# Kernel optimization log

Hardware: AMD Instinct MI355X
Metric: run time of the kernel (lower is better)

Reference implementation:

```python
import jax, jax.numpy as jnp
import numpy as np

WS = 7          # window size
SHIFT = 3       # shift size = ws // 2
HEADS = 16
N = WS * WS     # tokens per window


def _rel_pos_index(ws):
    coords = np.stack(np.meshgrid(np.arange(ws), np.arange(ws), indexing='ij')).reshape(2, -1)
    rel = (coords[:, :, None] - coords[:, None, :]).transpose(1, 2, 0)
    rel[:, :, 0] += ws - 1
    rel[:, :, 1] += ws - 1
    rel[:, :, 0] *= 2 * ws - 1
    return rel.sum(-1)  # [N, N] int


def _attn_mask(H, W, ws, s):
    # Swin cyclic-shift mask: windows spanning the wrap boundary get -100 on
    # cross-region pairs so softmax zeroes them out.
    img = np.zeros((H, W), np.float32)
    cnt = 0
    for hs in (slice(0, -ws), slice(-ws, -s), slice(-s, None)):
        for wsl in (slice(0, -ws), slice(-ws, -s), slice(-s, None)):
            img[hs, wsl] = cnt
            cnt += 1
    mw = img.reshape(H // ws, ws, W // ws, ws).transpose(0, 2, 1, 3).reshape(-1, ws * ws)
    diff = mw[:, None, :] - mw[:, :, None]
    return np.where(diff != 0, np.float32(-100.0), np.float32(0.0))  # [nW, N, N]


def _window_partition(x, ws):
    B, H, W, C = x.shape
    x = x.reshape(B, H // ws, ws, W // ws, ws, C).transpose(0, 1, 3, 2, 4, 5)
    return x.reshape(-1, ws * ws, C)  # [B*nW, N, C]


def _window_reverse(x, ws, B, H, W):
    C = x.shape[-1]
    x = x.reshape(B, H // ws, W // ws, ws, ws, C).transpose(0, 1, 3, 2, 4, 5)
    return x.reshape(B, H, W, C)


def setup_inputs() -> dict:
    key = jax.random.key(0)
    ks = jax.random.split(key, 5)
    B, H, W, C = 16, 56, 56, 512
    x = jax.random.normal(ks[0], (B, H, W, C), jnp.float32)
    qkv_w = jax.random.normal(ks[1], (C, 3 * C), jnp.float32) * 0.02
    qkv_b = jnp.zeros((3 * C,), jnp.float32)
    proj_w = jax.random.normal(ks[2], (C, C), jnp.float32) * 0.02
    proj_b = jnp.zeros((C,), jnp.float32)
    rel_bias_table = jax.random.normal(ks[3], ((2 * WS - 1) ** 2, HEADS), jnp.float32) * 0.02
    return {"x": x, "qkv_w": qkv_w, "qkv_b": qkv_b,
            "proj_w": proj_w, "proj_b": proj_b, "rel_bias_table": rel_bias_table}


def reference(x, qkv_w, qkv_b, proj_w, proj_b, rel_bias_table):
    B, H, W, C = x.shape
    d = C // HEADS
    scale = jnp.float32(d) ** -0.5

    rel_idx = jnp.asarray(_rel_pos_index(WS))                 # [N, N]
    mask = jnp.asarray(_attn_mask(H, W, WS, SHIFT))           # [nW, N, N]
    nW = mask.shape[0]

    shortcut = x
    # cyclic shift
    xs = jnp.roll(x, shift=(-SHIFT, -SHIFT), axis=(1, 2))
    xw = _window_partition(xs, WS)                            # [B*nW, N, C]

    qkv = xw @ qkv_w + qkv_b                                  # [B*nW, N, 3C]
    qkv = qkv.reshape(-1, N, 3, HEADS, d).transpose(2, 0, 3, 1, 4)
    q, k, v = qkv[0], qkv[1], qkv[2]                          # each [B*nW, h, N, d]

    attn = jnp.einsum('whnd,whmd->whnm', q * scale, k)        # [B*nW, h, N, N]
    # gathered relative-position bias [h, N, N]
    bias = rel_bias_table[rel_idx.reshape(-1)].reshape(N, N, HEADS).transpose(2, 0, 1)
    attn = attn + bias[None]
    # shift mask, broadcast per window
    attn = attn.reshape(B, nW, HEADS, N, N) + mask[None, :, None]
    attn = jax.nn.softmax(attn.reshape(-1, HEADS, N, N), axis=-1)

    out = jnp.einsum('whnm,whmd->whnd', attn, v)              # [B*nW, h, N, d]
    out = out.transpose(0, 2, 1, 3).reshape(-1, N, C)
    out = out @ proj_w + proj_b

    out = _window_reverse(out, WS, B, H, W)
    out = jnp.roll(out, shift=(SHIFT, SHIFT), axis=(1, 2))
    return shortcut + out
```

## Files before the change

### kernel.cpp

```cpp
#include <hip/hip_runtime.h>
#include <stdint.h>

typedef unsigned short u16;
typedef unsigned int   u32;

typedef __bf16 bf16x8 __attribute__((ext_vector_type(8)));
typedef float  f32x4  __attribute__((ext_vector_type(4)));

__device__ __forceinline__ float bf2f(u16 h) {
    return __uint_as_float(((u32)h) << 16);
}
__device__ __forceinline__ u16 f2bf(float f) {
    u32 u = __float_as_uint(f);
    u += 0x7FFFu + ((u >> 16) & 1u);
    return (u16)(u >> 16);
}

#define GLOAD_LDS16(g, l)                                                     \
    __builtin_amdgcn_global_load_lds(                                         \
        (const __attribute__((address_space(1))) void*)(g),                   \
        (__attribute__((address_space(3))) void*)(l), 16, 0, 0)

__global__ __launch_bounds__(256) void cvt_f32_bf16(const float* __restrict__ in,
                                                    u16* __restrict__ out) {
    int i = blockIdx.x * 256 + threadIdx.x;
    const float4* p = (const float4*)in + (size_t)i * 2;
    float4 a = p[0], b = p[1];
    union { u16 s[8]; uint4 v; } o;
    o.s[0] = f2bf(a.x); o.s[1] = f2bf(a.y); o.s[2] = f2bf(a.z); o.s[3] = f2bf(a.w);
    o.s[4] = f2bf(b.x); o.s[5] = f2bf(b.y); o.s[6] = f2bf(b.z); o.s[7] = f2bf(b.w);
    ((uint4*)out)[i] = o.v;
}

__global__ void transpose_cvt(const float* __restrict__ in, u16* __restrict__ out,
                              int R, int Cc) {
    __shared__ float tile[32][33];
    int c0 = blockIdx.x * 32, r0 = blockIdx.y * 32;
    int tx = threadIdx.x, ty = threadIdx.y;
    tile[ty][tx] = in[(size_t)(r0 + ty) * Cc + c0 + tx];
    __syncthreads();
    out[(size_t)(c0 + ty) * R + r0 + tx] = f2bf(tile[tx][ty]);
}

__global__ __launch_bounds__(64) void build_bias(const float* __restrict__ table,
                                                 float* __restrict__ biasL) {
    int cls = blockIdx.x >> 4;
    int h   = blockIdx.x & 15;
    int lane = threadIdx.x;
    int quad = lane >> 4, l16 = lane & 15;
    int eh = cls >> 1, ew = cls & 1;
    float* base = biasL + (size_t)(cls * 16 + h) * 4096;
#pragma unroll
    for (int mi = 0; mi < 4; mi++) {
#pragma unroll
        for (int ni = 0; ni < 4; ni++) {
            float4 v;
            float* vp = &v.x;
#pragma unroll
            for (int r = 0; r < 4; r++) {
                int m = mi * 16 + quad * 4 + r;
                int c = ni * 16 + l16;
                float b;
                if (c >= 49)      b = -1e9f;
                else if (m >= 49) b = 0.f;
                else {
                    int ty = m / 7, tx = m % 7, jy = c / 7, jx = c % 7;
                    b = table[((ty - jy + 6) * 13 + (tx - jx + 6)) * 16 + h];
                    int ridr = (eh ? (ty < 4 ? 1 : 2) : 0) * 3 + (ew ? (tx < 4 ? 1 : 2) : 0);
                    int ridc = (eh ? (jy < 4 ? 1 : 2) : 0) * 3 + (ew ? (jx < 4 ? 1 : 2) : 0);
                    if (ridr != ridc) b -= 100.f;
                }
                vp[r] = b;
            }
            ((float4*)base)[((mi * 4 + ni) * 4 + quad) * 16 + l16] = v;
        }
    }
}

template <bool OUT_F32>
__global__ __launch_bounds__(256) void gemm_bt(
    const u16* __restrict__ A, const u16* __restrict__ Bt,
    const float* __restrict__ bias, const float* __restrict__ res,
    void* __restrict__ Cout, int M, int N, int K)
{
    __shared__ __align__(16) char smem[17408];
    u16* As = (u16*)smem;
    u16* Bs = (u16*)(smem + 8192);

    const int t    = threadIdx.x;
    const int lane = t & 63;
    const int w    = t >> 6;
    const int wm   = w >> 1, wn = w & 1;
    const int quad = lane >> 4, l16 = lane & 15;

    const size_t m0 = (size_t)blockIdx.y * 128;
    const size_t n0 = (size_t)blockIdx.x * 128;

    const u16* Ab = A + m0 * K;
    const u16* Bb = Bt + n0 * K;

    const int rA0 = t >> 2;
    const int cA0 = (t & 3) * 8;

    f32x4 acc[4][4];
    const f32x4 fzero = {0.f, 0.f, 0.f, 0.f};
#pragma unroll
    for (int i = 0; i < 4; i++)
#pragma unroll
        for (int j = 0; j < 4; j++) acc[i][j] = fzero;

    for (int k0 = 0; k0 < K; k0 += 32) {
        const u16* ga0 = Ab + (size_t)rA0 * K + k0 + cA0;
        const u16* ga1 = ga0 + (size_t)64 * K;
        const u16* gb0 = Bb + (size_t)rA0 * K + k0 + cA0;
        const u16* gb1 = gb0 + (size_t)64 * K;
        GLOAD_LDS16(ga0, As + t * 8);
        GLOAD_LDS16(ga1, As + t * 8 + 2048);
        GLOAD_LDS16(gb0, Bs + t * 8);
        GLOAD_LDS16(gb1, Bs + t * 8 + 2048);
        __syncthreads();

        bf16x8 a[4], b[4];
#pragma unroll
        for (int mi = 0; mi < 4; mi++)
            a[mi] = *(const bf16x8*)(As + (wm * 64 + mi * 16 + l16) * 32 + quad * 8);
#pragma unroll
        for (int ni = 0; ni < 4; ni++)
            b[ni] = *(const bf16x8*)(Bs + (wn * 64 + ni * 16 + l16) * 32 + quad * 8);
#pragma unroll
        for (int mi = 0; mi < 4; mi++)
#pragma unroll
            for (int ni = 0; ni < 4; ni++)
                acc[mi][ni] = __builtin_amdgcn_mfma_f32_16x16x32_bf16(
                    a[mi], b[ni], acc[mi][ni], 0, 0, 0);
        __syncthreads();
    }

    float* scr = (float*)smem + w * 1088;
    float bv[4];
#pragma unroll
    for (int ni = 0; ni < 4; ni++)
        bv[ni] = bias[n0 + wn * 64 + ni * 16 + l16];

    const size_t colb = n0 + wn * 64 + quad * 16;
#pragma unroll
    for (int mi = 0; mi < 4; mi++) {
#pragma unroll
        for (int ni = 0; ni < 4; ni++)
#pragma unroll
            for (int r = 0; r < 4; r++)
                scr[(quad * 4 + r) * 68 + ni * 16 + l16] = acc[mi][ni][r] + bv[ni];
        __builtin_amdgcn_s_waitcnt(0);

        const size_t row = m0 + wm * 64 + mi * 16 + l16;
        const float4* sp = (const float4*)(scr + l16 * 68 + quad * 16);
        float4 v0 = sp[0], v1 = sp[1], v2 = sp[2], v3 = sp[3];

        if (OUT_F32) {
            const float4* rp = (const float4*)(res + row * N + colb);
            float4 r0 = rp[0], r1 = rp[1], r2 = rp[2], r3 = rp[3];
            v0.x += r0.x; v0.y += r0.y; v0.z += r0.z; v0.w += r0.w;
            v1.x += r1.x; v1.y += r1.y; v1.z += r1.z; v1.w += r1.w;
            v2.x += r2.x; v2.y += r2.y; v2.z += r2.z; v2.w += r2.w;
            v3.x += r3.x; v3.y += r3.y; v3.z += r3.z; v3.w += r3.w;
            float4* op = (float4*)((float*)Cout + row * N + colb);
            op[0] = v0; op[1] = v1; op[2] = v2; op[3] = v3;
        } else {
            union { u16 s[8]; uint4 q; } p0, p1;
            p0.s[0] = f2bf(v0.x); p0.s[1] = f2bf(v0.y); p0.s[2] = f2bf(v0.z); p0.s[3] = f2bf(v0.w);
            p0.s[4] = f2bf(v1.x); p0.s[5] = f2bf(v1.y); p0.s[6] = f2bf(v1.z); p0.s[7] = f2bf(v1.w);
            p1.s[0] = f2bf(v2.x); p1.s[1] = f2bf(v2.y); p1.s[2] = f2bf(v2.z); p1.s[3] = f2bf(v2.w);
            p1.s[4] = f2bf(v3.x); p1.s[5] = f2bf(v3.y); p1.s[6] = f2bf(v3.z); p1.s[7] = f2bf(v3.w);
            uint4* op = (uint4*)((u16*)Cout + row * N + colb);
            op[0] = p0.q; op[1] = p1.q;
        }
        __builtin_amdgcn_s_waitcnt(0);
    }
}

__global__ __launch_bounds__(64) void attn_kernel(
    const u16* __restrict__ qkv, const float* __restrict__ biasL,
    u16* __restrict__ O)
{
    __shared__ __align__(16) u16 Ps[64 * 72];
    __shared__ __align__(16) u16 Vts[32 * 72];

    const int wid = blockIdx.x >> 4;
    const int h   = blockIdx.x & 15;
    const int b   = wid >> 6;
    const int wy  = (wid >> 3) & 7;
    const int wx  = wid & 7;
    const int cls = ((wy == 7) ? 2 : 0) + ((wx == 7) ? 1 : 0);
    const int lane = threadIdx.x;
    const int quad = lane >> 4, l16 = lane & 15;

    auto tokOf = [&](int m) -> size_t {
        int tt = m < 49 ? m : 48;
        int ty = tt / 7, tx = tt - ty * 7;
        int ho = wy * 7 + ty + 3; if (ho >= 56) ho -= 56;
        int wo = wx * 7 + tx + 3; if (wo >= 56) wo -= 56;
        return ((size_t)b * 56 + ho) * 56 + wo;
    };

    {
        size_t tok = tokOf(lane);
        const uint4* vs = (const uint4*)(qkv + tok * 1536 + 1024 + h * 32);
        union { uint4 u4[4]; u16 s[32]; } vb;
        vb.u4[0] = vs[0]; vb.u4[1] = vs[1]; vb.u4[2] = vs[2]; vb.u4[3] = vs[3];
#pragma unroll
        for (int d = 0; d < 32; d++) Vts[d * 72 + lane] = vb.s[d];
    }

    bf16x8 aq[4], bk[4];
#pragma unroll
    for (int i = 0; i < 4; i++) {
        size_t tok = tokOf(i * 16 + l16);
        const u16* base = qkv + tok * 1536 + h * 32 + quad * 8;
        aq[i] = *(const bf16x8*)base;
        bk[i] = *(const bf16x8*)(base + 512);
    }

    f32x4 acc[4][4];
    {
        const f32x4 fz = {0.f, 0.f, 0.f, 0.f};
#pragma unroll
        for (int mi = 0; mi < 4; mi++)
#pragma unroll
            for (int ni = 0; ni < 4; ni++)
                acc[mi][ni] = __builtin_amdgcn_mfma_f32_16x16x32_bf16(
                    aq[mi], bk[ni], fz, 0, 0, 0);
    }

    {
        const float scale = 0.17677669529663687f;
        const float* bp = biasL + (size_t)(cls * 16 + h) * 4096;
#pragma unroll
        for (int mi = 0; mi < 4; mi++)
#pragma unroll
            for (int ni = 0; ni < 4; ni++) {
                float4 bvv = ((const float4*)bp)[((mi * 4 + ni) * 4 + quad) * 16 + l16];
                const float* bvp = &bvv.x;
#pragma unroll
                for (int r = 0; r < 4; r++)
                    acc[mi][ni][r] = acc[mi][ni][r] * scale + bvp[r];
            }
    }

    float rinv[4][4];
    {
#pragma unroll
        for (int mi = 0; mi < 4; mi++)
#pragma unroll
            for (int r = 0; r < 4; r++) {
                float m0 = fmaxf(fmaxf(acc[mi][0][r], acc[mi][1][r]),
                                 fmaxf(acc[mi][2][r], acc[mi][3][r]));
                m0 = fmaxf(m0, __shfl_xor(m0, 1, 64));
                m0 = fmaxf(m0, __shfl_xor(m0, 2, 64));
                m0 = fmaxf(m0, __shfl_xor(m0, 4, 64));
                m0 = fmaxf(m0, __shfl_xor(m0, 8, 64));
                float e0 = __expf(acc[mi][0][r] - m0);
                float e1 = __expf(acc[mi][1][r] - m0);
                float e2 = __expf(acc[mi][2][r] - m0);
                float e3 = __expf(acc[mi][3][r] - m0);
                acc[mi][0][r] = e0; acc[mi][1][r] = e1;
                acc[mi][2][r] = e2; acc[mi][3][r] = e3;
                float s0 = (e0 + e1) + (e2 + e3);
                s0 += __shfl_xor(s0, 1, 64);
                s0 += __shfl_xor(s0, 2, 64);
                s0 += __shfl_xor(s0, 4, 64);
                s0 += __shfl_xor(s0, 8, 64);
                rinv[mi][r] = __builtin_amdgcn_rcpf(s0);
            }
    }

#pragma unroll
    for (int mi = 0; mi < 4; mi++)
#pragma unroll
        for (int ni = 0; ni < 4; ni++)
#pragma unroll
            for (int r = 0; r < 4; r++)
                Ps[(mi * 16 + quad * 4 + r) * 72 + ni * 16 + l16] =
                    f2bf(acc[mi][ni][r]);
    __syncthreads();

#pragma unroll
    for (int mi = 0; mi < 4; mi++) {
        f32x4 c0 = {0.f, 0.f, 0.f, 0.f}, c1 = {0.f, 0.f, 0.f, 0.f};
#pragma unroll
        for (int ks = 0; ks < 2; ks++) {
            bf16x8 a = *(const bf16x8*)(Ps + (mi * 16 + l16) * 72 + ks * 32 + quad * 8);
            bf16x8 b0 = *(const bf16x8*)(Vts + l16 * 72 + ks * 32 + quad * 8);
            bf16x8 b1 = *(const bf16x8*)(Vts + (16 + l16) * 72 + ks * 32 + quad * 8);
            c0 = __builtin_amdgcn_mfma_f32_16x16x32_bf16(a, b0, c0, 0, 0, 0);
            c1 = __builtin_amdgcn_mfma_f32_16x16x32_bf16(a, b1, c1, 0, 0, 0);
        }
#pragma unroll
        for (int r = 0; r < 4; r++) {
            int m = mi * 16 + quad * 4 + r;
            if (m < 49) {
                int ty = m / 7, tx = m - ty * 7;
                int ho = wy * 7 + ty + 3; if (ho >= 56) ho -= 56;
                int wo = wx * 7 + tx + 3; if (wo >= 56) wo -= 56;
                size_t tok = ((size_t)b * 56 + ho) * 56 + wo;
                u16* op = O + tok * 512 + h * 32 + l16;
                op[0]  = f2bf(c0[r] * rinv[mi][r]);
                op[16] = f2bf(c1[r] * rinv[mi][r]);
            }
        }
    }
}

extern "C" void kernel_launch(void* const* d_in, const int* in_sizes, int n_in,
                              void* d_out, int out_size, void* d_ws, size_t ws_size,
                              hipStream_t stream)
{
    const float* x      = (const float*)d_in[0];
    const float* qkv_w  = (const float*)d_in[1];
    const float* qkv_b  = (const float*)d_in[2];
    const float* proj_w = (const float*)d_in[3];
    const float* proj_b = (const float*)d_in[4];
    const float* table  = (const float*)d_in[5];
    float* out = (float*)d_out;

    const int M  = 16 * 56 * 56;
    const int Cd = 512, C3 = 1536;

    char* ws = (char*)d_ws;
    u16* QKV  = (u16*)ws;
    u16* Xb   = (u16*)(ws + (size_t)M * C3 * 2);
    u16* Obuf = Xb;
    u16* Wt1  = (u16*)(ws + (size_t)M * C3 * 2 + (size_t)M * Cd * 2);
    u16* Wt2  = Wt1 + (size_t)C3 * Cd;
    float* biasL = (float*)Wt1;

    cvt_f32_bf16<<<(M * Cd) / 2048, 256, 0, stream>>>(x, Xb);

    dim3 tb(32, 32);
    transpose_cvt<<<dim3(C3 / 32, Cd / 32), tb, 0, stream>>>(qkv_w, Wt1, Cd, C3);
    transpose_cvt<<<dim3(Cd / 32, Cd / 32), tb, 0, stream>>>(proj_w, Wt2, Cd, Cd);

    gemm_bt<false><<<dim3(C3 / 128, M / 128), 256, 0, stream>>>(
        Xb, Wt1, qkv_b, nullptr, QKV, M, C3, Cd);

    build_bias<<<dim3(64), 64, 0, stream>>>(table, biasL);

    attn_kernel<<<dim3(1024 * 16), 64, 0, stream>>>(QKV, biasL, Obuf);

    gemm_bt<true><<<dim3(Cd / 128, M / 128), 256, 0, stream>>>(
        Obuf, Wt2, proj_b, x, out, M, Cd, Cd);
}
```

Measured before the change: 478.9 us.

## Replace 128x128 GEMM with double-buffered 256x256 swizzled pipelined GEMM

Replaces the simple single-buffered 128x128 bf16 GEMM with a 256x256-tile, 512-thread kernel that uses a 64-wide K step. It double-buffers LDS across half-tiles and interleaves global-to-LDS prefetch with MFMA phases under s_setprio. LDS reads use an XOR swizzle to avoid bank conflicts, and workgroup IDs are remapped for L2 locality. The goal is to hide load latency and raise arithmetic intensity for both the QKV and projection GEMMs. The cost is 128KB of LDS per block, which limits occupancy, and fragile manual vmcnt waits and barriers.

After: 453.7 us. -5.3%, faster.

```diff
diff --git a/kernel.cpp b/kernel.cpp
--- a/kernel.cpp
+++ b/kernel.cpp
@@ -78,91 +78,190 @@
 }
 
 template <bool OUT_F32>
-__global__ __launch_bounds__(256) void gemm_bt(
+__global__ __launch_bounds__(512, 2) void gemm256(
     const u16* __restrict__ A, const u16* __restrict__ Bt,
     const float* __restrict__ bias, const float* __restrict__ res,
-    void* __restrict__ Cout, int M, int N, int K)
+    void* __restrict__ Cout, int M, int N, int K, int GX)
 {
-    __shared__ __align__(16) char smem[17408];
-    u16* As = (u16*)smem;
-    u16* Bs = (u16*)(smem + 8192);
+    __shared__ __align__(16) char smem[131072];
+    char* AsB = smem;
+    char* BsB = smem + 65536;
+
+    const int nwg = (int)gridDim.x;
+    int wg = (int)blockIdx.x;
+    wg = (wg & 7) * (nwg >> 3) + (wg >> 3);
+    const int bx = wg % GX;
+    const int by = wg / GX;
+    const size_t m0 = (size_t)by * 256;
+    const size_t n0 = (size_t)bx * 256;
 
     const int t    = threadIdx.x;
     const int lane = t & 63;
     const int w    = t >> 6;
-    const int wm   = w >> 1, wn = w & 1;
+    const int wm   = w >> 2, wn = w & 3;
     const int quad = lane >> 4, l16 = lane & 15;
-
-    const size_t m0 = (size_t)blockIdx.y * 128;
-    const size_t n0 = (size_t)blockIdx.x * 128;
-
-    const u16* Ab = A + m0 * K;
-    const u16* Bb = Bt + n0 * K;
-
-    const int rA0 = t >> 2;
-    const int cA0 = (t & 3) * 8;
-
-    f32x4 acc[4][4];
-    const f32x4 fzero = {0.f, 0.f, 0.f, 0.f};
-#pragma unroll
-    for (int i = 0; i < 4; i++)
-#pragma unroll
-        for (int j = 0; j < 4; j++) acc[i][j] = fzero;
-
-    for (int k0 = 0; k0 < K; k0 += 32) {
-        const u16* ga0 = Ab + (size_t)rA0 * K + k0 + cA0;
-        const u16* ga1 = ga0 + (size_t)64 * K;
-        const u16* gb0 = Bb + (size_t)rA0 * K + k0 + cA0;
-        const u16* gb1 = gb0 + (size_t)64 * K;
-        GLOAD_LDS16(ga0, As + t * 8);
-        GLOAD_LDS16(ga1, As + t * 8 + 2048);
-        GLOAD_LDS16(gb0, Bs + t * 8);
-        GLOAD_LDS16(gb1, Bs + t * 8 + 2048);
-        __syncthreads();
-
-        bf16x8 a[4], b[4];
-#pragma unroll
-        for (int mi = 0; mi < 4; mi++)
-            a[mi] = *(const bf16x8*)(As + (wm * 64 + mi * 16 + l16) * 32 + quad * 8);
-#pragma unroll
-        for (int ni = 0; ni < 4; ni++)
-            b[ni] = *(const bf16x8*)(Bs + (wn * 64 + ni * 16 + l16) * 32 + quad * 8);
-#pragma unroll
-        for (int mi = 0; mi < 4; mi++)
-#pragma unroll
-            for (int ni = 0; ni < 4; ni++)
-                acc[mi][ni] = __builtin_amdgcn_mfma_f32_16x16x32_bf16(
-                    a[mi], b[ni], acc[mi][ni], 0, 0, 0);
-        __syncthreads();
-    }
-
-    float* scr = (float*)smem + w * 1088;
+    const int xr   = l16 & 7;
+    const int cb   = (quad ^ xr) * 16;
+
+    const int r0  = t >> 3;
+    const int s8  = t & 7;
+    const int swz = (s8 ^ (r0 & 7)) * 8;
+    const u16* Ag0 = A  + (m0 + r0) * K + swz;
+    const u16* Bg0 = Bt + (n0 + r0) * K + swz;
+    const size_t j64K = (size_t)64 * K;
+    const int lo0 = t * 16, lo1 = t * 16 + 8192;
+
+    auto stageA = [&](int bf, int half, int ktt) {
+        char* d = AsB + bf * 32768 + half * 16384;
+        const u16* g = Ag0 + (size_t)half * 128 * K + ktt * 64;
+        GLOAD_LDS16(g, d + lo0);
+        GLOAD_LDS16(g + j64K, d + lo1);
+    };
+    auto stageB = [&](int bf, int half, int ktt) {
+        char* d = BsB + bf * 32768 + half * 16384;
+        const u16* g = Bg0 + (size_t)half * 128 * K + ktt * 64;
+        GLOAD_LDS16(g, d + lo0);
+        GLOAD_LDS16(g + j64K, d + lo1);
+    };
+
+    f32x4 acc[8][4];
+    const f32x4 fz = {0.f, 0.f, 0.f, 0.f};
+#pragma unroll
+    for (int i = 0; i < 8; i++)
+#pragma unroll
+        for (int j = 0; j < 4; j++) acc[i][j] = fz;
+
+    const int NT = K >> 6;
+
+    stageA(0, 0, 0); stageA(0, 1, 0); stageB(0, 0, 0); stageB(0, 1, 0);
+    stageB(1, 0, 1); stageA(1, 0, 1);
+    asm volatile("s_waitcnt vmcnt(4)" ::: "memory");
+    __builtin_amdgcn_s_barrier();
+
+    for (int kt = 0; kt < NT; ++kt) {
+        const int buf = kt & 1;
+        const char* Ab  = AsB + buf * 32768 + wm * 16384 + l16 * 128;
+        const char* Bb  = BsB + buf * 32768 + (wn >> 1) * 16384 + (wn & 1) * 8192 + l16 * 128;
+        const char* pA0 = Ab + cb;
+        const char* pA1 = Ab + (cb ^ 64);
+        const char* pB0 = Bb + cb;
+        const char* pB1 = Bb + (cb ^ 64);
+
+        bf16x8 a[4][2], b0[2][2], b1[2][2];
+
+#pragma unroll
+        for (int mi = 0; mi < 4; mi++) {
+            a[mi][0] = *(const bf16x8*)(pA0 + mi * 2048);
+            a[mi][1] = *(const bf16x8*)(pA1 + mi * 2048);
+        }
+#pragma unroll
+        for (int nj = 0; nj < 2; nj++) {
+            b0[nj][0] = *(const bf16x8*)(pB0 + nj * 2048);
+            b0[nj][1] = *(const bf16x8*)(pB1 + nj * 2048);
+        }
+        if (kt + 1 < NT) stageA((kt + 1) & 1, 1, kt + 1);
+        __builtin_amdgcn_s_barrier();
+        asm volatile("s_waitcnt lgkmcnt(0)" ::: "memory");
+        __builtin_amdgcn_s_setprio(1);
+#pragma unroll
+        for (int mi = 0; mi < 4; mi++)
+#pragma unroll
+            for (int nj = 0; nj < 2; nj++) {
+                acc[mi][nj] = __builtin_amdgcn_mfma_f32_16x16x32_bf16(
+                    a[mi][0], b0[nj][0], acc[mi][nj], 0, 0, 0);
+                acc[mi][nj] = __builtin_amdgcn_mfma_f32_16x16x32_bf16(
+                    a[mi][1], b0[nj][1], acc[mi][nj], 0, 0, 0);
+            }
+        __builtin_amdgcn_s_setprio(0);
+        __builtin_amdgcn_s_barrier();
+
+#pragma unroll
+        for (int nj = 0; nj < 2; nj++) {
+            b1[nj][0] = *(const bf16x8*)(pB0 + 4096 + nj * 2048);
+            b1[nj][1] = *(const bf16x8*)(pB1 + 4096 + nj * 2048);
+        }
+        if (kt + 1 < NT) stageB((kt + 1) & 1, 1, kt + 1);
+        __builtin_amdgcn_s_barrier();
+        asm volatile("s_waitcnt lgkmcnt(0)" ::: "memory");
+        __builtin_amdgcn_s_setprio(1);
+#pragma unroll
+        for (int mi = 0; mi < 4; mi++)
+#pragma unroll
+            for (int nj = 0; nj < 2; nj++) {
+                acc[mi][2 + nj] = __builtin_amdgcn_mfma_f32_16x16x32_bf16(
+                    a[mi][0], b1[nj][0], acc[mi][2 + nj], 0, 0, 0);
+                acc[mi][2 + nj] = __builtin_amdgcn_mfma_f32_16x16x32_bf16(
+                    a[mi][1], b1[nj][1], acc[mi][2 + nj], 0, 0, 0);
+            }
+        __builtin_amdgcn_s_setprio(0);
+        __builtin_amdgcn_s_barrier();
+
+#pragma unroll
+        for (int mi = 0; mi < 4; mi++) {
+            a[mi][0] = *(const bf16x8*)(pA0 + 8192 + mi * 2048);
+            a[mi][1] = *(const bf16x8*)(pA1 + 8192 + mi * 2048);
+        }
+        if (kt + 2 < NT) stageB(buf, 0, kt + 2);
+        __builtin_amdgcn_s_barrier();
+        asm volatile("s_waitcnt lgkmcnt(0)" ::: "memory");
+        __builtin_amdgcn_s_setprio(1);
+#pragma unroll
+        for (int mi = 0; mi < 4; mi++)
+#pragma unroll
+            for (int nj = 0; nj < 2; nj++) {
+                acc[4 + mi][2 + nj] = __builtin_amdgcn_mfma_f32_16x16x32_bf16(
+                    a[mi][0], b1[nj][0], acc[4 + mi][2 + nj], 0, 0, 0);
+                acc[4 + mi][2 + nj] = __builtin_amdgcn_mfma_f32_16x16x32_bf16(
+                    a[mi][1], b1[nj][1], acc[4 + mi][2 + nj], 0, 0, 0);
+            }
+        __builtin_amdgcn_s_setprio(0);
+        __builtin_amdgcn_s_barrier();
+
+        if (kt + 2 < NT) stageA(buf, 0, kt + 2);
+        __builtin_amdgcn_s_barrier();
+        __builtin_amdgcn_s_setprio(1);
+#pragma unroll
+        for (int mi = 0; mi < 4; mi++)
+#pragma unroll
+            for (int nj = 0; nj < 2; nj++) {
+                acc[4 + mi][nj] = __builtin_amdgcn_mfma_f32_16x16x32_bf16(
+                    a[mi][0], b0[nj][0], acc[4 + mi][nj], 0, 0, 0);
+                acc[4 + mi][nj] = __builtin_amdgcn_mfma_f32_16x16x32_bf16(
+                    a[mi][1], b0[nj][1], acc[4 + mi][nj], 0, 0, 0);
+            }
+        __builtin_amdgcn_s_setprio(0);
+        if (kt < NT - 2) asm volatile("s_waitcnt vmcnt(4)" ::: "memory");
+        else             asm volatile("s_waitcnt vmcnt(0)" ::: "memory");
+        __builtin_amdgcn_s_barrier();
+    }
+
+    float* scr = (float*)(void*)smem + w * 1088;
     float bv[4];
 #pragma unroll
-    for (int ni = 0; ni < 4; ni++)
-        bv[ni] = bias[n0 + wn * 64 + ni * 16 + l16];
+    for (int nj = 0; nj < 4; nj++)
+        bv[nj] = bias[n0 + wn * 64 + nj * 16 + l16];
 
     const size_t colb = n0 + wn * 64 + quad * 16;
 #pragma unroll
-    for (int mi = 0; mi < 4; mi++) {
-#pragma unroll
-        for (int ni = 0; ni < 4; ni++)
+    for (int mi = 0; mi < 8; mi++) {
+#pragma unroll
+        for (int nj = 0; nj < 4; nj++)
 #pragma unroll
             for (int r = 0; r < 4; r++)
-                scr[(quad * 4 + r) * 68 + ni * 16 + l16] = acc[mi][ni][r] + bv[ni];
+                scr[(quad * 4 + r) * 68 + nj * 16 + l16] = acc[mi][nj][r] + bv[nj];
         __builtin_amdgcn_s_waitcnt(0);
 
-        const size_t row = m0 + wm * 64 + mi * 16 + l16;
+        const size_t row = m0 + wm * 128 + mi * 16 + l16;
         const float4* sp = (const float4*)(scr + l16 * 68 + quad * 16);
         float4 v0 = sp[0], v1 = sp[1], v2 = sp[2], v3 = sp[3];
 
         if (OUT_F32) {
             const float4* rp = (const float4*)(res + row * N + colb);
-            float4 r0 = rp[0], r1 = rp[1], r2 = rp[2], r3 = rp[3];
-            v0.x += r0.x; v0.y += r0.y; v0.z += r0.z; v0.w += r0.w;
-            v1.x += r1.x; v1.y += r1.y; v1.z += r1.z; v1.w += r1.w;
-            v2.x += r2.x; v2.y += r2.y; v2.z += r2.z; v2.w += r2.w;
-            v3.x += r3.x; v3.y += r3.y; v3.z += r3.z; v3.w += r3.w;
+            float4 r0v = rp[0], r1v = rp[1], r2v = rp[2], r3v = rp[3];
+            v0.x += r0v.x; v0.y += r0v.y; v0.z += r0v.z; v0.w += r0v.w;
+            v1.x += r1v.x; v1.y += r1v.y; v1.z += r1v.z; v1.w += r1v.w;
+            v2.x += r2v.x; v2.y += r2v.y; v2.z += r2v.z; v2.w += r2v.w;
+            v3.x += r3v.x; v3.y += r3v.y; v3.z += r3v.z; v3.w += r3v.w;
             float4* op = (float4*)((float*)Cout + row * N + colb);
             op[0] = v0; op[1] = v1; op[2] = v2; op[3] = v3;
         } else {
@@ -222,13 +321,13 @@
 
     f32x4 acc[4][4];
     {
-        const f32x4 fz = {0.f, 0.f, 0.f, 0.f};
+        const f32x4 fzz = {0.f, 0.f, 0.f, 0.f};
 #pragma unroll
         for (int mi = 0; mi < 4; mi++)
 #pragma unroll
             for (int ni = 0; ni < 4; ni++)
                 acc[mi][ni] = __builtin_amdgcn_mfma_f32_16x16x32_bf16(
-                    aq[mi], bk[ni], fz, 0, 0, 0);
+                    aq[mi], bk[ni], fzz, 0, 0, 0);
     }
 
     {
@@ -339,13 +438,13 @@
     transpose_cvt<<<dim3(C3 / 32, Cd / 32), tb, 0, stream>>>(qkv_w, Wt1, Cd, C3);
     transpose_cvt<<<dim3(Cd / 32, Cd / 32), tb, 0, stream>>>(proj_w, Wt2, Cd, Cd);
 
-    gemm_bt<false><<<dim3(C3 / 128, M / 128), 256, 0, stream>>>(
-        Xb, Wt1, qkv_b, nullptr, QKV, M, C3, Cd);
+    gemm256<false><<<dim3((M / 256) * (C3 / 256)), 512, 0, stream>>>(
+        Xb, Wt1, qkv_b, nullptr, QKV, M, C3, Cd, C3 / 256);
 
     build_bias<<<dim3(64), 64, 0, stream>>>(table, biasL);
 
     attn_kernel<<<dim3(1024 * 16), 64, 0, stream>>>(QKV, biasL, Obuf);
 
-    gemm_bt<true><<<dim3(Cd / 128, M / 128), 256, 0, stream>>>(
-        Obuf, Wt2, proj_b, x, out, M, Cd, Cd);
-}
+    gemm256<true><<<dim3((M / 256) * (Cd / 256)), 512, 0, stream>>>(
+        Obuf, Wt2, proj_b, x, out, M, Cd, Cd, Cd / 256);
+}
```
